# Kernel optimization log

Hardware: AMD Instinct MI355X
Metric: run time of the kernel (lower is better)

The kernel has to match this reference:

```python
import jax, jax.numpy as jnp
import numpy as np

NUM_HEADS = 16

def setup_inputs() -> dict:
    key = jax.random.key(0)
    ks = jax.random.split(key, 5)
    B, T, C = 2, 2048, 1024
    s = 0.02
    return {
        "x": jax.random.normal(ks[0], (B, T, C), dtype=jnp.float32),
        "attn_w": jax.random.normal(ks[1], (3 * C, C), dtype=jnp.float32) * s,
        "attn_b": jax.random.normal(ks[2], (3 * C,), dtype=jnp.float32) * s,
        "proj_w": jax.random.normal(ks[3], (C, C), dtype=jnp.float32) * s,
        "proj_b": jax.random.normal(ks[4], (C,), dtype=jnp.float32) * s,
    }

def reference(x, attn_w, attn_b, proj_w, proj_b):
    B, T, C = x.shape
    H = NUM_HEADS
    D = C // H
    # fused QKV projection (torch Linear: x @ W^T + b)
    qkv = x @ attn_w.T + attn_b                      # [B, T, 3C]
    q, k, v = jnp.split(qkv, 3, axis=-1)             # each [B, T, C]
    # split heads -> [B, H, T, D]
    def heads(t):
        return t.reshape(B, T, H, D).transpose(0, 2, 1, 3)
    q, k, v = heads(q), heads(k), heads(v)
    scale = 1.0 / jnp.sqrt(jnp.asarray(D, dtype=x.dtype))
    scores = jnp.einsum("bhtd,bhsd->bhts", q, k) * scale   # [B, H, T, T]
    causal = jnp.tril(jnp.ones((T, T), dtype=bool))
    scores = jnp.where(causal[None, None], scores, jnp.asarray(-jnp.inf, dtype=scores.dtype))
    att = jax.nn.softmax(scores, axis=-1)
    out = jnp.einsum("bhts,bhsd->bhtd", att, v)      # [B, H, T, D]
    out = out.transpose(0, 2, 1, 3).reshape(B, T, C)
    return out @ proj_w.T + proj_b
```

## Files before the change

kernel.cpp:

```cpp
#include <hip/hip_runtime.h>
#include <hip/hip_bf16.h>

typedef __bf16 bf16_t;
typedef __bf16 bf16x4 __attribute__((ext_vector_type(4)));
typedef __bf16 bf16x8 __attribute__((ext_vector_type(8)));
typedef float f32x4 __attribute__((ext_vector_type(4)));
typedef float f32x8 __attribute__((ext_vector_type(8)));

#define MFMA16(a, b, c) __builtin_amdgcn_mfma_f32_16x16x32_bf16(a, b, c, 0, 0, 0)

#define GLOAD_LDS16(g, l)                                              \
  __builtin_amdgcn_global_load_lds(                                    \
      (const __attribute__((address_space(1))) unsigned int*)(g),      \
      (__attribute__((address_space(3))) unsigned int*)(l), 16, 0, 0)

constexpr int B = 2, T = 2048, C = 1024, H = 16, D = 64;
constexpr int NQKV = 3 * C;
constexpr int M = B * T;

__global__ __launch_bounds__(256) void cvt_kernel(
    const float* __restrict__ s0, bf16_t* __restrict__ d0, int n0,
    const float* __restrict__ s1, bf16_t* __restrict__ d1, int n1,
    const float* __restrict__ s2, bf16_t* __restrict__ d2, int n2)
{
  const float* s; bf16_t* d; int n;
  if (blockIdx.y == 0)      { s = s0; d = d0; n = n0; }
  else if (blockIdx.y == 1) { s = s1; d = d1; n = n1; }
  else                      { s = s2; d = d2; n = n2; }
  const int idx = (blockIdx.x * 256 + threadIdx.x) * 8;
  if (idx >= n) return;
  f32x8 t = *(const f32x8*)(s + idx);
  bf16x8 r;
#pragma unroll
  for (int j = 0; j < 8; ++j) r[j] = (bf16_t)t[j];
  *(bf16x8*)(d + idx) = r;
}

template<int BN, int NI>
__device__ __forceinline__ void gemm_mainloop_db(
    const bf16_t* __restrict__ A, const bf16_t* __restrict__ Wt,
    const int K, const int m0, const int n0,
    bf16_t* ldsA0, bf16_t* ldsA1, bf16_t* ldsB0, bf16_t* ldsB1,
    f32x4 acc[4][NI])
{
  const int tid  = threadIdx.x;
  const int wv   = tid >> 6;
  const int lane = tid & 63;
  const int col  = lane & 15;
  const int quad = lane >> 4;
  const int lr8  = lane >> 3;
  const int cpos = lane & 7;
  const int wm = wv >> 1, wn = wv & 1;
  constexpr int BJ = BN / 32;
  constexpr int BRW = BN / 4;

  const bf16_t* ag[4]; const bf16_t* bg[BJ];
#pragma unroll
  for (int j = 0; j < 4; ++j)
    ag[j] = A + (size_t)(m0 + wv * 32 + j * 8 + lr8) * K + (cpos ^ lr8) * 8;
#pragma unroll
  for (int j = 0; j < BJ; ++j)
    bg[j] = Wt + (size_t)(n0 + wv * BRW + j * 8 + lr8) * K + (cpos ^ lr8) * 8;

  const int xa = quad ^ (col & 7);
  const int niter = K / 64;

#pragma unroll
  for (int j = 0; j < 4; ++j)
    GLOAD_LDS16(ag[j], ldsA0 + (wv * 32 + j * 8) * 64);
#pragma unroll
  for (int j = 0; j < BJ; ++j)
    GLOAD_LDS16(bg[j], ldsB0 + (wv * BRW + j * 8) * 64);

  for (int it = 0; it < niter; ++it) {
    __syncthreads();
    const bf16_t* cA = (it & 1) ? ldsA1 : ldsA0;
    const bf16_t* cB = (it & 1) ? ldsB1 : ldsB0;
    if (it + 1 < niter) {
      bf16_t* nA = (it & 1) ? ldsA0 : ldsA1;
      bf16_t* nB = (it & 1) ? ldsB0 : ldsB1;
      const int off = (it + 1) * 64;
#pragma unroll
      for (int j = 0; j < 4; ++j)
        GLOAD_LDS16(ag[j] + off, nA + (wv * 32 + j * 8) * 64);
#pragma unroll
      for (int j = 0; j < BJ; ++j)
        GLOAD_LDS16(bg[j] + off, nB + (wv * BRW + j * 8) * 64);
    }
#pragma unroll
    for (int ks = 0; ks < 2; ++ks) {
      const int xk = (xa ^ (ks * 4)) * 8;
      bf16x8 af[4], bfr[NI];
#pragma unroll
      for (int mi = 0; mi < 4; ++mi)
        af[mi] = *(const bf16x8*)(cA + (wm * 64 + mi * 16 + col) * 64 + xk);
#pragma unroll
      for (int ni = 0; ni < NI; ++ni)
        bfr[ni] = *(const bf16x8*)(cB + (wn * (NI * 16) + ni * 16 + col) * 64 + xk);
#pragma unroll
      for (int mi = 0; mi < 4; ++mi)
#pragma unroll
        for (int ni = 0; ni < NI; ++ni)
          acc[mi][ni] = MFMA16(af[mi], bfr[ni], acc[mi][ni]);
    }
  }
}

__global__ __launch_bounds__(256) void qkv_gemm_kernel(
    const bf16_t* __restrict__ x, const bf16_t* __restrict__ w,
    const float* __restrict__ bias,
    bf16_t* __restrict__ qws, bf16_t* __restrict__ kws, bf16_t* __restrict__ vws)
{
  __shared__ __align__(16) bf16_t ldsA[2][128 * 64];
  __shared__ __align__(16) bf16_t ldsB[2][128 * 64];
  const int lane = threadIdx.x & 63;
  const int wv   = threadIdx.x >> 6;
  const int col  = lane & 15;
  const int quad = lane >> 4;
  const int wm = wv >> 1, wn = wv & 1;
  const int m0 = blockIdx.y * 128;
  const int n0 = blockIdx.x * 128;

  f32x4 acc[4][4] = {};
  gemm_mainloop_db<128, 4>(x, w, C, m0, n0,
                           ldsA[0], ldsA[1], ldsB[0], ldsB[1], acc);

  const int which = n0 >> 10;

  if (which == 2) {
    __syncthreads();
    bf16_t* vt = &ldsA[0][0] + wv * 4096;

#pragma unroll
    for (int ni = 0; ni < 4; ++ni) {
      const int n = n0 + wn * 64 + ni * 16 + col;
      const float bval = bias[n];
      const int d = n & 63;
#pragma unroll
      for (int r = 0; r < 4; ++r) {
        bf16x4 pw;
#pragma unroll
        for (int mi = 0; mi < 4; ++mi)
          pw[mi] = (bf16_t)(acc[mi][ni][r] + bval);
        const int k = 2 * quad + (r >> 1);
        const int S = d * 8 + (k ^ (d & 7));
        *(bf16x4*)(vt + S * 8 + (r & 1) * 4) = pw;
      }
    }

    const int b   = (m0 + wm * 64) >> 11;
    const int t0w = (m0 + wm * 64) & (T - 1);
    const int h   = ((n0 & (C - 1)) + wn * 64) >> 6;
    const size_t bh = (size_t)(b * H + h);
    const int lr8 = lane >> 3;
    const int c8  = lane & 7;
#pragma unroll
    for (int j = 0; j < 8; ++j) {
      const int d = j * 8 + lr8;
      bf16x8 row = *(const bf16x8*)(vt + (d * 8 + (c8 ^ (d & 7))) * 8);
      *(bf16x8*)(vws + (bh * D + d) * T + t0w + c8 * 8) = row;
    }
  } else {
#pragma unroll
    for (int ni = 0; ni < 4; ++ni) {
      const int n = n0 + wn * 64 + ni * 16 + col;
      const float bval = bias[n];
      const int c = n & (C - 1);
      const int h = c >> 6;
      const int d = c & 63;
#pragma unroll
      for (int mi = 0; mi < 4; ++mi) {
#pragma unroll
        for (int r = 0; r < 4; ++r) {
          const int m = m0 + wm * 64 + mi * 16 + quad * 4 + r;
          const int b = m >> 11;
          const int t = m & (T - 1);
          const bf16_t bv = (bf16_t)(acc[mi][ni][r] + bval);
          const size_t bh = (size_t)(b * H + h);
          if (which == 0) qws[(bh * T + t) * D + d] = bv;
          else            kws[(bh * T + t) * D + d] = bv;
        }
      }
    }
  }
}

__global__ __launch_bounds__(256) void attn_kernel(
    const bf16_t* __restrict__ qws, const bf16_t* __restrict__ kws,
    const bf16_t* __restrict__ vws, bf16_t* __restrict__ yws)
{
  const int id = blockIdx.x;
  const int bh = id & 31;
  const int pr = id >> 5;
  const int tid  = threadIdx.x;
  const int wv   = tid >> 6;
  const int lane = tid & 63;
  const int col  = lane & 15;
  const int quad = lane >> 4;

  const bf16_t* Q  = qws + (size_t)bh * T * D;
  const bf16_t* K  = kws + (size_t)bh * T * D;
  const bf16_t* Vt = vws + (size_t)bh * D * T;

  __shared__ __align__(16) bf16_t ldsK[2][64 * 64];
  __shared__ __align__(16) bf16_t ldsV[2][64 * 64];
  __shared__ __align__(16) bf16_t ldsP[4][16 * 64];
  bf16_t* ldsPw = ldsP[wv];

  const float cscale = 0.125f * 1.44269504088896340736f;

  const int xs   = col & 7;
  const int cxq  = (quad ^ xs) * 8;
  const int lr8  = lane >> 3;
  const int ksrc = (lane & 7) ^ lr8;
  const int pxor = (quad & 1) * 4;
  const int b = bh >> 4;
  const int h = bh & 15;

  const int qt_h = 31 - pr, qt_l = pr;
  const int t0h = qt_h * 64, t0l = qt_l * 64;
  const int twh = t0h + 16 * wv, twl = t0l + 16 * wv;
  const int niter = qt_h + 1;

  bf16x8 qfh0 = *(const bf16x8*)(Q + (size_t)(twh + col) * D + quad * 8);
  bf16x8 qfh1 = *(const bf16x8*)(Q + (size_t)(twh + col) * D + 32 + quad * 8);
  bf16x8 qfl0 = *(const bf16x8*)(Q + (size_t)(twl + col) * D + quad * 8);
  bf16x8 qfl1 = *(const bf16x8*)(Q + (size_t)(twl + col) * D + 32 + quad * 8);

  f32x4 oh[4] = {}, ol[4] = {};
  f32x4 lph = {}, lpl = {};

  auto compute_tile = [&](const bf16_t* bK, const bf16_t* bV, int s0, int tw,
                          int t0, bf16x8 qf0, bf16x8 qf1,
                          f32x4 (&o)[4], f32x4& lp) {
    f32x4 sc[4];
#pragma unroll
    for (int kb = 0; kb < 4; ++kb) {
      const bf16_t* kr = bK + (kb * 16 + col) * 64;
      bf16x8 kf0 = *(const bf16x8*)(kr + cxq);
      bf16x8 kf1 = *(const bf16x8*)(kr + (cxq ^ 32));
      f32x4 a = {};
      a = MFMA16(qf0, kf0, a);
      a = MFMA16(qf1, kf1, a);
      sc[kb] = a;
    }
    const bool diag = (s0 == t0);
#pragma unroll
    for (int r = 0; r < 4; ++r) {
      const int prow = (quad * 4 + r) * 64;
      const int pxr  = pxor + r;
      bf16x4 pw;
#pragma unroll
      for (int kb = 0; kb < 4; ++kb) {
        float p = __builtin_amdgcn_exp2f(sc[kb][r] * cscale);
        if (diag && (s0 + kb * 16 + col > tw + quad * 4 + r)) p = 0.0f;
        lp[r] += p;
        pw[kb] = (bf16_t)p;
      }
      *(bf16x4*)(ldsPw + prow + (((col >> 1) ^ pxr) * 8) + (col & 1) * 4) = pw;
    }
#pragma unroll
    for (int ks = 0; ks < 2; ++ks) {
      const int xk = cxq ^ (ks * 32);
      bf16x8 pa = *(const bf16x8*)(ldsPw + col * 64 + xk);
#pragma unroll
      for (int ni = 0; ni < 4; ++ni) {
        bf16x8 vf = *(const bf16x8*)(bV + (ni * 16 + col) * 64 + xk);
        o[ni] = MFMA16(pa, vf, o[ni]);
      }
    }
  };

#pragma unroll
  for (int j = 0; j < 2; ++j) {
    GLOAD_LDS16(K + (size_t)(16 * wv + j * 8 + lr8) * D + ksrc * 8,
                ldsK[0] + (16 * wv + j * 8) * 64);
    GLOAD_LDS16(Vt + (size_t)(16 * wv + j * 8 + lr8) * T + ksrc * 8,
                ldsV[0] + (16 * wv + j * 8) * 64);
  }

  for (int it = 0; it < niter; ++it) {
    const int s0 = it * 64;
    __syncthreads();

    if (it + 1 < niter) {
      const int sn = s0 + 64;
      bf16_t* dK = ldsK[(it + 1) & 1];
      bf16_t* dV = ldsV[(it + 1) & 1];
#pragma unroll
      for (int j = 0; j < 2; ++j) {
        GLOAD_LDS16(K + (size_t)(sn + 16 * wv + j * 8 + lr8) * D + ksrc * 8,
                    dK + (16 * wv + j * 8) * 64);
        GLOAD_LDS16(Vt + (size_t)(16 * wv + j * 8 + lr8) * T + sn + ksrc * 8,
                    dV + (16 * wv + j * 8) * 64);
      }
    }

    const bf16_t* bK = ldsK[it & 1];
    const bf16_t* bV = ldsV[it & 1];

    compute_tile(bK, bV, s0, twh, t0h, qfh0, qfh1, oh, lph);
    if (s0 <= t0l)
      compute_tile(bK, bV, s0, twl, t0l, qfl0, qfl1, ol, lpl);
  }

#pragma unroll
  for (int r = 0; r < 4; ++r) {
    float l0 = lph[r], l1 = lpl[r];
#pragma unroll
    for (int off = 1; off < 16; off <<= 1) {
      l0 += __shfl_xor(l0, off);
      l1 += __shfl_xor(l1, off);
    }
    const float rl0 = 1.0f / l0, rl1 = 1.0f / l1;
    const int th = twh + quad * 4 + r;
    const int tl = twl + quad * 4 + r;
#pragma unroll
    for (int ni = 0; ni < 4; ++ni) {
      const int d = ni * 16 + col;
      yws[((size_t)(b * T + th)) * C + h * D + d] = (bf16_t)(oh[ni][r] * rl0);
      yws[((size_t)(b * T + tl)) * C + h * D + d] = (bf16_t)(ol[ni][r] * rl1);
    }
  }
}

__global__ __launch_bounds__(256) void proj_gemm_kernel(
    const bf16_t* __restrict__ y, const bf16_t* __restrict__ w,
    const float* __restrict__ bias, float* __restrict__ out)
{
  __shared__ __align__(16) bf16_t ldsA[2][128 * 64];
  __shared__ __align__(16) bf16_t ldsB[2][64 * 64];
  const int lane = threadIdx.x & 63;
  const int wv   = threadIdx.x >> 6;
  const int col  = lane & 15;
  const int quad = lane >> 4;
  const int wm = wv >> 1, wn = wv & 1;
  const int m0 = blockIdx.y * 128;
  const int n0 = blockIdx.x * 64;

  f32x4 acc[4][2] = {};
  gemm_mainloop_db<64, 2>(y, w, C, m0, n0,
                          ldsA[0], ldsA[1], ldsB[0], ldsB[1], acc);

#pragma unroll
  for (int ni = 0; ni < 2; ++ni) {
    const int n = n0 + wn * 32 + ni * 16 + col;
    const float bval = bias[n];
#pragma unroll
    for (int mi = 0; mi < 4; ++mi) {
#pragma unroll
      for (int r = 0; r < 4; ++r) {
        const int m = m0 + wm * 64 + mi * 16 + quad * 4 + r;
        out[(size_t)m * C + n] = acc[mi][ni][r] + bval;
      }
    }
  }
}

extern "C" void kernel_launch(void* const* d_in, const int* in_sizes, int n_in,
                              void* d_out, int out_size, void* d_ws, size_t ws_size,
                              hipStream_t stream) {
  const float* x      = (const float*)d_in[0];
  const float* attn_w = (const float*)d_in[1];
  const float* attn_b = (const float*)d_in[2];
  const float* proj_w = (const float*)d_in[3];
  const float* proj_b = (const float*)d_in[4];
  float* out = (float*)d_out;

  const size_t E = (size_t)B * H * T * D;
  char* ws = (char*)d_ws;
  bf16_t* qws = (bf16_t*)(ws);
  bf16_t* kws = (bf16_t*)(ws + 2 * E);
  bf16_t* vws = (bf16_t*)(ws + 4 * E);
  bf16_t* yws = (bf16_t*)(ws + 6 * E);
  bf16_t* xb  = (bf16_t*)(ws + 8 * E);
  bf16_t* awb = (bf16_t*)(ws + 10 * E);
  bf16_t* pwb = (bf16_t*)(ws + 11 * E + E / 2);

  const int NX = M * C, NAW = NQKV * C, NPW = C * C;
  cvt_kernel<<<dim3(NX / 2048, 3), 256, 0, stream>>>(
      x, xb, NX, attn_w, awb, NAW, proj_w, pwb, NPW);
  qkv_gemm_kernel<<<dim3(NQKV / 128, M / 128), 256, 0, stream>>>(
      xb, awb, attn_b, qws, kws, vws);
  attn_kernel<<<512, 256, 0, stream>>>(qws, kws, vws, yws);
  proj_gemm_kernel<<<dim3(C / 64, M / 128), 256, 0, stream>>>(
      yws, pwb, proj_b, out);
}
```

Baseline: 169.2 us.

## Fold softmax scale into Q, split diagonal masking path, shrink proj GEMM tile

The softmax scale (1/sqrt(D)·log2e) is folded into Q in the QKV GEMM epilogue, which removes a multiply per score in the attention inner loop. The attention P computation is split into diagonal and off-diagonal branches so the mask compare runs only on the diagonal tile. The projection GEMM tile drops from 128x64 to 64x64, doubling the block count (1024 blocks) for better CU occupancy, at the cost of less data reuse per block. Rounding Q to bf16 after scaling slightly changes numerics.

```diff
diff --git a/kernel.cpp b/kernel.cpp
--- a/kernel.cpp
+++ b/kernel.cpp
@@ -17,6 +17,8 @@
 constexpr int B = 2, T = 2048, C = 1024, H = 16, D = 64;
 constexpr int NQKV = 3 * C;
 constexpr int M = B * T;
+
+#define QSCALE 0.18033688011112042f
 
 __global__ __launch_bounds__(256) void cvt_kernel(
     const float* __restrict__ s0, bf16_t* __restrict__ d0, int n0,
@@ -36,12 +38,12 @@
   *(bf16x8*)(d + idx) = r;
 }
 
-template<int BN, int NI>
+template<int BM, int BN, int MI, int NI>
 __device__ __forceinline__ void gemm_mainloop_db(
     const bf16_t* __restrict__ A, const bf16_t* __restrict__ Wt,
     const int K, const int m0, const int n0,
     bf16_t* ldsA0, bf16_t* ldsA1, bf16_t* ldsB0, bf16_t* ldsB1,
-    f32x4 acc[4][NI])
+    f32x4 acc[MI][NI])
 {
   const int tid  = threadIdx.x;
   const int wv   = tid >> 6;
@@ -51,13 +53,15 @@
   const int lr8  = lane >> 3;
   const int cpos = lane & 7;
   const int wm = wv >> 1, wn = wv & 1;
+  constexpr int AJ = BM / 32;
+  constexpr int ARW = BM / 4;
   constexpr int BJ = BN / 32;
   constexpr int BRW = BN / 4;
 
-  const bf16_t* ag[4]; const bf16_t* bg[BJ];
-#pragma unroll
-  for (int j = 0; j < 4; ++j)
-    ag[j] = A + (size_t)(m0 + wv * 32 + j * 8 + lr8) * K + (cpos ^ lr8) * 8;
+  const bf16_t* ag[AJ]; const bf16_t* bg[BJ];
+#pragma unroll
+  for (int j = 0; j < AJ; ++j)
+    ag[j] = A + (size_t)(m0 + wv * ARW + j * 8 + lr8) * K + (cpos ^ lr8) * 8;
 #pragma unroll
   for (int j = 0; j < BJ; ++j)
     bg[j] = Wt + (size_t)(n0 + wv * BRW + j * 8 + lr8) * K + (cpos ^ lr8) * 8;
@@ -66,8 +70,8 @@
   const int niter = K / 64;
 
 #pragma unroll
-  for (int j = 0; j < 4; ++j)
-    GLOAD_LDS16(ag[j], ldsA0 + (wv * 32 + j * 8) * 64);
+  for (int j = 0; j < AJ; ++j)
+    GLOAD_LDS16(ag[j], ldsA0 + (wv * ARW + j * 8) * 64);
 #pragma unroll
   for (int j = 0; j < BJ; ++j)
     GLOAD_LDS16(bg[j], ldsB0 + (wv * BRW + j * 8) * 64);
@@ -81,8 +85,8 @@
       bf16_t* nB = (it & 1) ? ldsB0 : ldsB1;
       const int off = (it + 1) * 64;
 #pragma unroll
-      for (int j = 0; j < 4; ++j)
-        GLOAD_LDS16(ag[j] + off, nA + (wv * 32 + j * 8) * 64);
+      for (int j = 0; j < AJ; ++j)
+        GLOAD_LDS16(ag[j] + off, nA + (wv * ARW + j * 8) * 64);
 #pragma unroll
       for (int j = 0; j < BJ; ++j)
         GLOAD_LDS16(bg[j] + off, nB + (wv * BRW + j * 8) * 64);
@@ -90,15 +94,15 @@
 #pragma unroll
     for (int ks = 0; ks < 2; ++ks) {
       const int xk = (xa ^ (ks * 4)) * 8;
-      bf16x8 af[4], bfr[NI];
-#pragma unroll
-      for (int mi = 0; mi < 4; ++mi)
-        af[mi] = *(const bf16x8*)(cA + (wm * 64 + mi * 16 + col) * 64 + xk);
+      bf16x8 af[MI], bfr[NI];
+#pragma unroll
+      for (int mi = 0; mi < MI; ++mi)
+        af[mi] = *(const bf16x8*)(cA + (wm * (MI * 16) + mi * 16 + col) * 64 + xk);
 #pragma unroll
       for (int ni = 0; ni < NI; ++ni)
         bfr[ni] = *(const bf16x8*)(cB + (wn * (NI * 16) + ni * 16 + col) * 64 + xk);
 #pragma unroll
-      for (int mi = 0; mi < 4; ++mi)
+      for (int mi = 0; mi < MI; ++mi)
 #pragma unroll
         for (int ni = 0; ni < NI; ++ni)
           acc[mi][ni] = MFMA16(af[mi], bfr[ni], acc[mi][ni]);
@@ -122,8 +126,8 @@
   const int n0 = blockIdx.x * 128;
 
   f32x4 acc[4][4] = {};
-  gemm_mainloop_db<128, 4>(x, w, C, m0, n0,
-                           ldsA[0], ldsA[1], ldsB[0], ldsB[1], acc);
+  gemm_mainloop_db<128, 128, 4, 4>(x, w, C, m0, n0,
+                                   ldsA[0], ldsA[1], ldsB[0], ldsB[1], acc);
 
   const int which = n0 >> 10;
 
@@ -175,10 +179,11 @@
           const int m = m0 + wm * 64 + mi * 16 + quad * 4 + r;
           const int b = m >> 11;
           const int t = m & (T - 1);
-          const bf16_t bv = (bf16_t)(acc[mi][ni][r] + bval);
           const size_t bh = (size_t)(b * H + h);
-          if (which == 0) qws[(bh * T + t) * D + d] = bv;
-          else            kws[(bh * T + t) * D + d] = bv;
+          if (which == 0)
+            qws[(bh * T + t) * D + d] = (bf16_t)((acc[mi][ni][r] + bval) * QSCALE);
+          else
+            kws[(bh * T + t) * D + d] = (bf16_t)(acc[mi][ni][r] + bval);
         }
       }
     }
@@ -207,8 +212,6 @@
   __shared__ __align__(16) bf16_t ldsP[4][16 * 64];
   bf16_t* ldsPw = ldsP[wv];
 
-  const float cscale = 0.125f * 1.44269504088896340736f;
-
   const int xs   = col & 7;
   const int cxq  = (quad ^ xs) * 8;
   const int lr8  = lane >> 3;
@@ -244,20 +247,35 @@
       a = MFMA16(qf1, kf1, a);
       sc[kb] = a;
     }
-    const bool diag = (s0 == t0);
-#pragma unroll
-    for (int r = 0; r < 4; ++r) {
-      const int prow = (quad * 4 + r) * 64;
-      const int pxr  = pxor + r;
-      bf16x4 pw;
-#pragma unroll
-      for (int kb = 0; kb < 4; ++kb) {
-        float p = __builtin_amdgcn_exp2f(sc[kb][r] * cscale);
-        if (diag && (s0 + kb * 16 + col > tw + quad * 4 + r)) p = 0.0f;
-        lp[r] += p;
-        pw[kb] = (bf16_t)p;
-      }
-      *(bf16x4*)(ldsPw + prow + (((col >> 1) ^ pxr) * 8) + (col & 1) * 4) = pw;
+    if (s0 == t0) {
+#pragma unroll
+      for (int r = 0; r < 4; ++r) {
+        const int prow = (quad * 4 + r) * 64;
+        const int pxr  = pxor + r;
+        bf16x4 pw;
+#pragma unroll
+        for (int kb = 0; kb < 4; ++kb) {
+          float p = __builtin_amdgcn_exp2f(sc[kb][r]);
+          if (s0 + kb * 16 + col > tw + quad * 4 + r) p = 0.0f;
+          lp[r] += p;
+          pw[kb] = (bf16_t)p;
+        }
+        *(bf16x4*)(ldsPw + prow + (((col >> 1) ^ pxr) * 8) + (col & 1) * 4) = pw;
+      }
+    } else {
+#pragma unroll
+      for (int r = 0; r < 4; ++r) {
+        const int prow = (quad * 4 + r) * 64;
+        const int pxr  = pxor + r;
+        bf16x4 pw;
+#pragma unroll
+        for (int kb = 0; kb < 4; ++kb) {
+          float p = __builtin_amdgcn_exp2f(sc[kb][r]);
+          lp[r] += p;
+          pw[kb] = (bf16_t)p;
+        }
+        *(bf16x4*)(ldsPw + prow + (((col >> 1) ^ pxr) * 8) + (col & 1) * 4) = pw;
+      }
     }
 #pragma unroll
     for (int ks = 0; ks < 2; ++ks) {
@@ -328,29 +346,29 @@
     const bf16_t* __restrict__ y, const bf16_t* __restrict__ w,
     const float* __restrict__ bias, float* __restrict__ out)
 {
-  __shared__ __align__(16) bf16_t ldsA[2][128 * 64];
+  __shared__ __align__(16) bf16_t ldsA[2][64 * 64];
   __shared__ __align__(16) bf16_t ldsB[2][64 * 64];
   const int lane = threadIdx.x & 63;
   const int wv   = threadIdx.x >> 6;
   const int col  = lane & 15;
   const int quad = lane >> 4;
   const int wm = wv >> 1, wn = wv & 1;
-  const int m0 = blockIdx.y * 128;
+  const int m0 = blockIdx.y * 64;
   const int n0 = blockIdx.x * 64;
 
-  f32x4 acc[4][2] = {};
-  gemm_mainloop_db<64, 2>(y, w, C, m0, n0,
-                          ldsA[0], ldsA[1], ldsB[0], ldsB[1], acc);
+  f32x4 acc[2][2] = {};
+  gemm_mainloop_db<64, 64, 2, 2>(y, w, C, m0, n0,
+                                 ldsA[0], ldsA[1], ldsB[0], ldsB[1], acc);
 
 #pragma unroll
   for (int ni = 0; ni < 2; ++ni) {
     const int n = n0 + wn * 32 + ni * 16 + col;
     const float bval = bias[n];
 #pragma unroll
-    for (int mi = 0; mi < 4; ++mi) {
+    for (int mi = 0; mi < 2; ++mi) {
 #pragma unroll
       for (int r = 0; r < 4; ++r) {
-        const int m = m0 + wm * 64 + mi * 16 + quad * 4 + r;
+        const int m = m0 + wm * 32 + mi * 16 + quad * 4 + r;
         out[(size_t)m * C + n] = acc[mi][ni][r] + bval;
       }
     }
@@ -383,6 +401,6 @@
   qkv_gemm_kernel<<<dim3(NQKV / 128, M / 128), 256, 0, stream>>>(
       xb, awb, attn_b, qws, kws, vws);
   attn_kernel<<<512, 256, 0, stream>>>(qws, kws, vws, yws);
-  proj_gemm_kernel<<<dim3(C / 64, M / 128), 256, 0, stream>>>(
+  proj_gemm_kernel<<<dim3(C / 64, M / 64), 256, 0, stream>>>(
       yws, pwb, proj_b, out);
 }
```

Result: no change. 170.0 us (+0.5%).
